# Kernel tuning notes

Measured on AMD Instinct MI355X. Metric: run time of the kernel, lower is better.

Reference implementation:

```python
import jax, jax.numpy as jnp
import numpy as np

# footprints from the module: RB = 8-neighbor ring (center excluded), G = 4-neighbor cross
RB_OFFSETS = [(-1, -1), (-1, 0), (-1, 1), (0, -1), (0, 1), (1, -1), (1, 0), (1, 1)]
G_OFFSETS = [(-1, 0), (0, -1), (0, 1), (1, 0)]
N_ITER = 3


def _footprint_median(x, offsets):
    """scipy.ndimage.median_filter with a boolean footprint.
    scipy uses rank = n//2 of the sorted footprint values (no averaging for even n)
    and 'reflect' boundary mode (== numpy 'symmetric' padding).
    x: [B, H, W]
    """
    B, H, W = x.shape
    xp = jnp.pad(x, ((0, 0), (1, 1), (1, 1)), mode='symmetric')
    vals = jnp.stack([xp[:, 1 + dy:1 + dy + H, 1 + dx:1 + dx + W]
                      for dy, dx in offsets], axis=0)  # [n, B, H, W]
    n = len(offsets)
    return jnp.sort(vals, axis=0)[n // 2]


def _conv3(x, k):
    """3x3 conv with symmetric padding. x: [B,H,W], k: [3,3] -> [B,H,W]."""
    xp = jnp.pad(x, ((0, 0), (1, 1), (1, 1)), mode='symmetric')[:, None]  # [B,1,H+2,W+2]
    kern = k[None, None].astype(x.dtype)  # [1,1,3,3]
    out = jax.lax.conv_general_dilated(xp, kern, (1, 1), 'VALID')
    return out[:, 0]


def _demosaick(x):
    """Naive bilinear demosaick of a GRBG Bayer mosaic. x: [B,H,W] -> [B,3,H,W]."""
    B, H, W = x.shape
    yy, xx = jnp.meshgrid(jnp.arange(H), jnp.arange(W), indexing='ij')
    r_mask = ((yy % 2 == 0) & (xx % 2 == 1)).astype(x.dtype)
    b_mask = ((yy % 2 == 1) & (xx % 2 == 0)).astype(x.dtype)
    g_mask = 1.0 - r_mask - b_mask
    KG = jnp.array([[0., 1., 0.], [1., 4., 1.], [0., 1., 0.]]) / 4.0
    KRB = jnp.array([[1., 2., 1.], [2., 4., 2.], [1., 2., 1.]]) / 4.0
    R = _conv3(x * r_mask, KRB)
    G = _conv3(x * g_mask, KG)
    Bc = _conv3(x * b_mask, KRB)
    return jnp.stack([R, G, Bc], axis=1)


def reference(image):
    # image: [B, 1, H, W] Bayer mosaic
    d = _demosaick(image[:, 0])  # [B, 3, H, W]
    R, G, B = d[:, 0], d[:, 1], d[:, 2]
    for _ in range(N_ITER):
        # medians are non-differentiable in the original (numpy roundtrip)
        R = jax.lax.stop_gradient(_footprint_median(R - G, RB_OFFSETS)) + G
        B = jax.lax.stop_gradient(_footprint_median(B - G, RB_OFFSETS)) + G
        G = 0.5 * (jax.lax.stop_gradient(_footprint_median(G - R, G_OFFSETS))
                   + jax.lax.stop_gradient(_footprint_median(G - B, G_OFFSETS))
                   + R + B)
    return jnp.stack([R, G, B], axis=1)


def setup_inputs() -> dict:
    key = jax.random.key(0)
    image = jax.random.uniform(key, (8, 1, 1024, 1024), dtype=jnp.float32)
    return {"image": image}
```

## Files before the change

### kernel.cpp

```cpp
#include <hip/hip_runtime.h>

#define HH 1024
#define WW 1024
#define NB 8
constexpr int PLANE = HH * WW;

#define S   84
#define RG  78
#define NTHR 1024

typedef _Float16 h2 __attribute__((ext_vector_type(2)));

__device__ __forceinline__ int clampi(int v, int lo, int hi) {
    return v < lo ? lo : (v > hi ? hi : v);
}

union U2H { unsigned u; h2 h; };
__device__ __forceinline__ h2 u2h(unsigned v) { U2H x; x.u = v; return x.h; }
__device__ __forceinline__ unsigned h2u(h2 h) { U2H x; x.h = h; return x.u; }
__device__ __forceinline__ unsigned packdiff(float a, float b) {
    h2 h; h.x = (_Float16)a; h.y = (_Float16)b; return h2u(h);
}
__device__ __forceinline__ h2 swap16(h2 x) {
    unsigned u = h2u(x);
    return u2h(__builtin_amdgcn_alignbit(u, u, 16));
}

__device__ __forceinline__ void cswap2(h2& a, h2& b) {
    h2 lo = __builtin_elementwise_min(a, b);
    b = __builtin_elementwise_max(a, b);
    a = lo;
}

__device__ __forceinline__ h2 med8p(h2 v0, h2 v1, h2 v2, h2 v3,
                                    h2 v4, h2 v5, h2 v6, h2 v7) {
    cswap2(v0, v1); cswap2(v2, v3); cswap2(v4, v5); cswap2(v6, v7);
    cswap2(v0, v2); cswap2(v1, v3); cswap2(v4, v6); cswap2(v5, v7);
    cswap2(v1, v2); cswap2(v5, v6);
    h2 p2 = __builtin_elementwise_min(v2, v6), p3 = __builtin_elementwise_min(v3, v7);
    h2 p4 = __builtin_elementwise_max(v0, v4), p5 = __builtin_elementwise_max(v1, v5);
    return __builtin_elementwise_max(__builtin_elementwise_min(p3, p5),
                                     __builtin_elementwise_max(p2, p4));
}

__device__ __forceinline__ h2 med4p(h2 a, h2 b, h2 c, h2 d) {
    h2 ab_hi = __builtin_elementwise_max(a, b), ab_lo = __builtin_elementwise_min(a, b);
    h2 cd_hi = __builtin_elementwise_max(c, d), cd_lo = __builtin_elementwise_min(c, d);
    return __builtin_elementwise_max(__builtin_elementwise_min(ab_hi, cd_hi),
                                     __builtin_elementwise_max(ab_lo, cd_lo));
}

__device__ __forceinline__ void demo_acc(float v, int pyn, int pxn, int ady, int adx,
                                         float& accR, float& accG, float& accB) {
    bool isr = (pyn == 0) && (pxn == 1);
    bool isb = (pyn == 1) && (pxn == 0);
    float wrb = 0.25f * (float)((2 - ady) * (2 - adx));
    int man = ady + adx;
    float wg = (man == 0) ? 1.0f : ((man == 1) ? 0.25f : 0.0f);
    accR += isr ? wrb * v : 0.0f;
    accB += isb ? wrb * v : 0.0f;
    accG += (!isr && !isb) ? wg * v : 0.0f;
}

template <int CA>
__device__ __forceinline__ void load4u(const unsigned* row, int c0, unsigned w[4]) {
    if constexpr (CA == 0) {
        uint4 q = *reinterpret_cast<const uint4*>(row + c0);
        w[0] = q.x; w[1] = q.y; w[2] = q.z; w[3] = q.w;
    } else {
        uint2 a = *reinterpret_cast<const uint2*>(row + c0);
        uint2 b = *reinterpret_cast<const uint2*>(row + c0 + 2);
        w[0] = a.x; w[1] = a.y; w[2] = b.x; w[3] = b.y;
    }
}
template <int CA>
__device__ __forceinline__ void load6u(const unsigned* row, int c0, unsigned w[6]) {
    if constexpr (CA == 0) {
        uint4 q = *reinterpret_cast<const uint4*>(row + c0);
        w[0] = row[c0 - 1];
        w[1] = q.x; w[2] = q.y; w[3] = q.z; w[4] = q.w;
        w[5] = row[c0 + 4];
    } else {
        uint4 a = *reinterpret_cast<const uint4*>(row + c0 - 2);
        uint4 b = *reinterpret_cast<const uint4*>(row + c0 + 2);
        w[0] = a.y; w[1] = a.z; w[2] = a.w; w[3] = b.x; w[4] = b.y; w[5] = b.z;
    }
}
template <int CA>
__device__ __forceinline__ void store4u(unsigned* row, int c0, const unsigned v[4]) {
    if constexpr (CA == 0) {
        *reinterpret_cast<uint4*>(row + c0) = make_uint4(v[0], v[1], v[2], v[3]);
    } else {
        *reinterpret_cast<uint2*>(row + c0) = make_uint2(v[0], v[1]);
        *reinterpret_cast<uint2*>(row + c0 + 2) = make_uint2(v[2], v[3]);
    }
}

template <int R0, int NRP, int C0, int NG>
__device__ __forceinline__ void p1_int(const unsigned* __restrict__ sdRB,
                                       unsigned* __restrict__ uRB, int tid) {
    static_assert((C0 & 3) == 2, "p1_int needs C0 % 4 == 2");
    if (tid < NRP * NG) {
        int rp = tid / NG, g = tid - rp * NG;
        int r0 = R0 + 2 * rp;
        int c0 = C0 + 4 * g;
        int B = c0 - 2;
        unsigned w[4][6];
#pragma unroll
        for (int i = 0; i < 4; ++i) {
            const unsigned* row = &sdRB[(r0 - 1 + i) * S + B];
            uint4 q0 = *reinterpret_cast<const uint4*>(row);
            uint4 q1 = *reinterpret_cast<const uint4*>(row + 4);
            w[i][0] = q0.y; w[i][1] = q0.z; w[i][2] = q0.w;
            w[i][3] = q1.x; w[i][4] = q1.y; w[i][5] = q1.z;
        }
#pragma unroll
        for (int rr = 0; rr < 2; ++rr) {
            unsigned rv[4];
#pragma unroll
            for (int i = 0; i < 4; ++i) {
                h2 m = med8p(u2h(w[rr][i]), u2h(w[rr][i + 1]), u2h(w[rr][i + 2]),
                             u2h(w[rr + 1][i]), u2h(w[rr + 1][i + 2]),
                             u2h(w[rr + 2][i]), u2h(w[rr + 2][i + 1]), u2h(w[rr + 2][i + 2]));
                rv[i] = h2u(-m);
            }
            store4u<2>(&uRB[(r0 + rr) * S], c0, rv);
        }
    }
}

template <int R0, int NRP, int C0, int NG, int CA, bool FINAL>
__device__ __forceinline__ void p2_int(_Float16* __restrict__ sG, unsigned* __restrict__ sdRB,
                                       const unsigned* __restrict__ uRB, int tid,
                                       int y0, int x0,
                                       float* __restrict__ oR, float* __restrict__ oG,
                                       float* __restrict__ oB) {
    if (tid < NRP * NG) {
        int rp = tid / NG, g = tid - rp * NG;
        int r0 = R0 + 2 * rp;
        int c0 = C0 + 4 * g;
        unsigned wm[4], wp[4], w0[6], w1[6];
        load4u<CA>(&uRB[(r0 - 1) * S], c0, wm);
        load6u<CA>(&uRB[(r0) * S], c0, w0);
        load6u<CA>(&uRB[(r0 + 1) * S], c0, w1);
        load4u<CA>(&uRB[(r0 + 2) * S], c0, wp);
        h2 ga0 = *reinterpret_cast<const h2*>(&sG[r0 * S + c0]);
        h2 ga1 = *reinterpret_cast<const h2*>(&sG[r0 * S + c0 + 2]);
        h2 gb0 = *reinterpret_cast<const h2*>(&sG[(r0 + 1) * S + c0]);
        h2 gb1 = *reinterpret_cast<const h2*>(&sG[(r0 + 1) * S + c0 + 2]);
        _Float16 gr0[4] = {ga0.x, ga0.y, ga1.x, ga1.y};
        _Float16 gr1[4] = {gb0.x, gb0.y, gb1.x, gb1.y};
        const h2 half2v = {(_Float16)0.5f, (_Float16)0.5f};

        unsigned nd0[4], nd1[4];
        float R4[2][4], G4[2][4], B4[2][4];
#pragma unroll
        for (int i = 0; i < 4; ++i) {
            {
                h2 m = med4p(u2h(wm[i]), u2h(w0[i]), u2h(w0[i + 2]), u2h(w1[i + 1]));
                h2 uc = u2h(w0[i + 1]);
                h2 gg; gg.x = gr0[i]; gg.y = gr0[i];
                h2 RB = gg - uc;
                h2 Gn2 = ((m + swap16(m)) + (RB + swap16(RB))) * half2v;
                if constexpr (FINAL) {
                    R4[0][i] = (float)RB.x; B4[0][i] = (float)RB.y; G4[0][i] = (float)Gn2.x;
                } else {
                    nd0[i] = h2u(RB - Gn2);
                    gr0[i] = Gn2.x;
                }
            }
            {
                h2 m = med4p(u2h(w0[i + 1]), u2h(w1[i]), u2h(w1[i + 2]), u2h(wp[i]));
                h2 uc = u2h(w1[i + 1]);
                h2 gg; gg.x = gr1[i]; gg.y = gr1[i];
                h2 RB = gg - uc;
                h2 Gn2 = ((m + swap16(m)) + (RB + swap16(RB))) * half2v;
                if constexpr (FINAL) {
                    R4[1][i] = (float)RB.x; B4[1][i] = (float)RB.y; G4[1][i] = (float)Gn2.x;
                } else {
                    nd1[i] = h2u(RB - Gn2);
                    gr1[i] = Gn2.x;
                }
            }
        }
        if constexpr (FINAL) {
#pragma unroll
            for (int rr = 0; rr < 2; ++rr) {
                size_t o = (size_t)(y0 + r0 + rr) * WW + (x0 + c0);
                *reinterpret_cast<float4*>(&oR[o]) = make_float4(R4[rr][0], R4[rr][1], R4[rr][2], R4[rr][3]);
                *reinterpret_cast<float4*>(&oG[o]) = make_float4(G4[rr][0], G4[rr][1], G4[rr][2], G4[rr][3]);
                *reinterpret_cast<float4*>(&oB[o]) = make_float4(B4[rr][0], B4[rr][1], B4[rr][2], B4[rr][3]);
            }
        } else {
            h2 s00; s00.x = gr0[0]; s00.y = gr0[1];
            h2 s01; s01.x = gr0[2]; s01.y = gr0[3];
            h2 s10; s10.x = gr1[0]; s10.y = gr1[1];
            h2 s11; s11.x = gr1[2]; s11.y = gr1[3];
            *reinterpret_cast<h2*>(&sG[r0 * S + c0]) = s00;
            *reinterpret_cast<h2*>(&sG[r0 * S + c0 + 2]) = s01;
            *reinterpret_cast<h2*>(&sG[(r0 + 1) * S + c0]) = s10;
            *reinterpret_cast<h2*>(&sG[(r0 + 1) * S + c0 + 2]) = s11;
            store4u<CA>(&sdRB[r0 * S], c0, nd0);
            store4u<CA>(&sdRB[(r0 + 1) * S], c0, nd1);
        }
    }
}

__device__ void p1_b(const unsigned* sdRB, unsigned* uRB, int tid,
                     int y0, int x0, int rlo, int nr, int clo, int nc) {
    for (int t = tid; t < nr * nc; t += NTHR) {
        int r = rlo + t / nc, c = clo + t - (t / nc) * nc;
        int gy = clampi(y0 + r, 0, HH - 1), gx = clampi(x0 + c, 0, WW - 1);
        int rm = clampi(gy - 1, 0, HH - 1) - y0, rp = clampi(gy + 1, 0, HH - 1) - y0;
        int cm = clampi(gx - 1, 0, WW - 1) - x0, cp = clampi(gx + 1, 0, WW - 1) - x0;
        h2 m = med8p(u2h(sdRB[rm * S + cm]), u2h(sdRB[rm * S + c]), u2h(sdRB[rm * S + cp]),
                     u2h(sdRB[r * S + cm]), u2h(sdRB[r * S + cp]),
                     u2h(sdRB[rp * S + cm]), u2h(sdRB[rp * S + c]), u2h(sdRB[rp * S + cp]));
        uRB[r * S + c] = h2u(-m);
    }
}

__device__ void p2_b(_Float16* sG, unsigned* sdRB, const unsigned* uRB, int tid,
                     int y0, int x0, int rlo, int nr, int clo, int nc, bool fin,
                     float* oR, float* oG, float* oB) {
    for (int t = tid; t < nr * nc; t += NTHR) {
        int r = rlo + t / nc, c = clo + t - (t / nc) * nc;
        int gy = clampi(y0 + r, 0, HH - 1), gx = clampi(x0 + c, 0, WW - 1);
        int rm = clampi(gy - 1, 0, HH - 1) - y0, rp = clampi(gy + 1, 0, HH - 1) - y0;
        int cm = clampi(gx - 1, 0, WW - 1) - x0, cp = clampi(gx + 1, 0, WW - 1) - x0;
        h2 m = med4p(u2h(uRB[rm * S + c]), u2h(uRB[r * S + cm]),
                     u2h(uRB[r * S + cp]), u2h(uRB[rp * S + c]));
        h2 uc = u2h(uRB[r * S + c]);
        float Gc = (float)sG[r * S + c];
        float Rn = Gc - (float)uc.x, Bn = Gc - (float)uc.y;
        float Gn = 0.5f * ((float)m.x + (float)m.y + Rn + Bn);
        if (fin) {
            size_t o = (size_t)(y0 + r) * WW + (x0 + c);
            oR[o] = Rn; oG[o] = Gn; oB[o] = Bn;
        } else {
            sG[r * S + c] = (_Float16)Gn;
            sdRB[r * S + c] = packdiff(Rn - Gn, Bn - Gn);
        }
    }
}

__global__ __launch_bounds__(1024) void fused_kernel(const float* __restrict__ img,
                                                     float* __restrict__ dst) {
    __shared__ __align__(16) unsigned smem[16380];
    unsigned* uRB = smem;
    unsigned* sdRB = smem + RG * S;
    _Float16* sG = reinterpret_cast<_Float16*>(smem + 2 * RG * S);
    float* sI = reinterpret_cast<float*>(smem);

    int bx = blockIdx.x, by = blockIdx.y, bb = blockIdx.z;
    int x0 = bx * 64 - 8, y0 = by * 64 - 7;
    const float* im = img + (size_t)bb * PLANE;
    float* oR = dst + (size_t)bb * 3 * PLANE;
    float* oG = oR + PLANE;
    float* oB = oR + 2 * PLANE;
    int tid = threadIdx.x;
    bool interior = (bx >= 1 && bx <= 14 && by >= 1 && by <= 14);

    if (interior) {
        if (tid < 38 * 19) {
            int qi = tid / 19, g = tid - (tid / 19) * 19;
            int rA = 1 + 2 * qi;
            int B = 4 * g;
            const float* base = im + (size_t)(y0 + rA - 1) * WW + (x0 + B);
            float w[4][6];
#pragma unroll
            for (int i = 0; i < 4; ++i) {
                float4 a = *reinterpret_cast<const float4*>(base + (size_t)i * WW);
                float4 b = *reinterpret_cast<const float4*>(base + (size_t)i * WW + 4);
                w[i][0] = a.y; w[i][1] = a.z; w[i][2] = a.w;
                w[i][3] = b.x; w[i][4] = b.y; w[i][5] = b.z;
            }
#pragma unroll
            for (int q = 0; q < 2; ++q) {
                int jb = 1 + 2 * q;
                float g00 = w[1][jb];
                float r00 = 0.5f * (w[1][jb - 1] + w[1][jb + 1]);
                float b00 = 0.5f * (w[0][jb] + w[2][jb]);
                float r01 = w[1][jb + 1];
                float g01 = 0.25f * (w[0][jb + 1] + w[2][jb + 1] + w[1][jb] + w[1][jb + 2]);
                float b01 = 0.25f * (w[0][jb] + w[0][jb + 2] + w[2][jb] + w[2][jb + 2]);
                float b10 = w[2][jb];
                float g10 = 0.25f * (w[1][jb] + w[3][jb] + w[2][jb - 1] + w[2][jb + 1]);
                float r10 = 0.25f * (w[1][jb - 1] + w[1][jb + 1] + w[3][jb - 1] + w[3][jb + 1]);
                float g11 = w[2][jb + 1];
                float r11 = 0.5f * (w[1][jb + 1] + w[3][jb + 1]);
                float b11 = 0.5f * (w[2][jb] + w[2][jb + 2]);
                int a0 = rA * S + 2 + 4 * g + 2 * q;
                h2 gh0; gh0.x = (_Float16)g00; gh0.y = (_Float16)g01;
                h2 gh1; gh1.x = (_Float16)g10; gh1.y = (_Float16)g11;
                *reinterpret_cast<h2*>(&sG[a0]) = gh0;
                *reinterpret_cast<h2*>(&sG[a0 + S]) = gh1;
                *reinterpret_cast<uint2*>(&sdRB[a0]) =
                    make_uint2(packdiff(r00 - g00, b00 - g00), packdiff(r01 - g01, b01 - g01));
                *reinterpret_cast<uint2*>(&sdRB[a0 + S]) =
                    make_uint2(packdiff(r10 - g10, b10 - g10), packdiff(r11 - g11, b11 - g11));
            }
        }
        __syncthreads();
        p1_int<2, 37, 2, 19>(sdRB, uRB, tid);
        __syncthreads();
        p2_int<3, 36, 4, 18, 0, false>(sG, sdRB, uRB, tid, y0, x0, oR, oG, oB);
        __syncthreads();
        p1_int<4, 35, 2, 19>(sdRB, uRB, tid);
        __syncthreads();
        p2_int<5, 34, 6, 17, 2, false>(sG, sdRB, uRB, tid, y0, x0, oR, oG, oB);
        __syncthreads();
        p1_int<6, 33, 6, 17>(sdRB, uRB, tid);
        __syncthreads();
        p2_int<7, 32, 8, 16, 0, true>(sG, sdRB, uRB, tid, y0, x0, oR, oG, oB);
    } else {
        for (int t = tid; t < RG * S; t += NTHR) {
            int r = t / S, c = t - (t / S) * S;
            int gy = clampi(y0 + r, 0, HH - 1), gx = clampi(x0 + c, 0, WW - 1);
            sI[r * S + c] = im[(size_t)gy * WW + gx];
        }
        __syncthreads();
        {
            for (int t = tid; t < 76 * 76; t += NTHR) {
                int r = 1 + t / 76, c = 2 + t - (t / 76) * 76;
                int gy = clampi(y0 + r, 0, HH - 1), gx = clampi(x0 + c, 0, WW - 1);
                float accR = 0.f, accG = 0.f, accB = 0.f;
#pragma unroll
                for (int dy = -1; dy <= 1; ++dy)
#pragma unroll
                    for (int dx = -1; dx <= 1; ++dx) {
                        int cy = clampi(gy + dy, 0, HH - 1);
                        int cx = clampi(gx + dx, 0, WW - 1);
                        float v = sI[(cy - y0) * S + (cx - x0)];
                        demo_acc(v, cy & 1, cx & 1, dy < 0 ? -dy : dy, dx < 0 ? -dx : dx,
                                 accR, accG, accB);
                    }
                sG[r * S + c] = (_Float16)accG;
                sdRB[r * S + c] = packdiff(accR - accG, accB - accG);
            }
        }
        __syncthreads();
        p1_b(sdRB, uRB, tid, y0, x0, 2, 74, 3, 74);
        __syncthreads();
        p2_b(sG, sdRB, uRB, tid, y0, x0, 3, 72, 4, 72, false, oR, oG, oB);
        __syncthreads();
        p1_b(sdRB, uRB, tid, y0, x0, 4, 70, 5, 70);
        __syncthreads();
        p2_b(sG, sdRB, uRB, tid, y0, x0, 5, 68, 6, 68, false, oR, oG, oB);
        __syncthreads();
        p1_b(sdRB, uRB, tid, y0, x0, 6, 66, 7, 66);
        __syncthreads();
        p2_b(sG, sdRB, uRB, tid, y0, x0, 7, 64, 8, 64, true, oR, oG, oB);
    }
}

extern "C" void kernel_launch(void* const* d_in, const int* in_sizes, int n_in,
                              void* d_out, int out_size, void* d_ws, size_t ws_size,
                              hipStream_t stream) {
    const float* img = (const float*)d_in[0];
    float* out = (float*)d_out;
    dim3 block(NTHR);
    dim3 grid(16, 16, NB);
    fused_kernel<<<grid, block, 0, stream>>>(img, out);
}
```

Before: 130.7 us.

## Vectorize border-tile path using interior quad kernels with scalar fallback for clamped cells

Border tiles previously ran a fully scalar per-pixel path for demosaick and all six median passes, with clamped neighbour indexing on every cell. The new code runs the vectorized interior routines on border tiles too, masking their stores to in-image cells, and recomputes only the out-of-image cells with a scalar per-cell routine that applies reflection clamping. Demosaick on border tiles likewise uses the quad routine wherever the 4x6 window is fully inside the image. This targets the slower border blocks (about a quarter of the grid), at the cost of extra branching, a second scalar pass, and more code size and register use.

```diff
diff --git a/kernel.cpp b/kernel.cpp
--- a/kernel.cpp
+++ b/kernel.cpp
@@ -60,6 +60,35 @@
     accR += isr ? wrb * v : 0.0f;
     accB += isb ? wrb * v : 0.0f;
     accG += (!isr && !isb) ? wg * v : 0.0f;
+}
+
+__device__ __forceinline__ void demo_quads2(const float w[4][6], unsigned* __restrict__ sdRB,
+                                            _Float16* __restrict__ sG, int a0base) {
+#pragma unroll
+    for (int q = 0; q < 2; ++q) {
+        int jb = 1 + 2 * q;
+        float g00 = w[1][jb];
+        float r00 = 0.5f * (w[1][jb - 1] + w[1][jb + 1]);
+        float b00 = 0.5f * (w[0][jb] + w[2][jb]);
+        float r01 = w[1][jb + 1];
+        float g01 = 0.25f * (w[0][jb + 1] + w[2][jb + 1] + w[1][jb] + w[1][jb + 2]);
+        float b01 = 0.25f * (w[0][jb] + w[0][jb + 2] + w[2][jb] + w[2][jb + 2]);
+        float b10 = w[2][jb];
+        float g10 = 0.25f * (w[1][jb] + w[3][jb] + w[2][jb - 1] + w[2][jb + 1]);
+        float r10 = 0.25f * (w[1][jb - 1] + w[1][jb + 1] + w[3][jb - 1] + w[3][jb + 1]);
+        float g11 = w[2][jb + 1];
+        float r11 = 0.5f * (w[1][jb + 1] + w[3][jb + 1]);
+        float b11 = 0.5f * (w[2][jb] + w[2][jb + 2]);
+        int a0 = a0base + 2 * q;
+        h2 gh0; gh0.x = (_Float16)g00; gh0.y = (_Float16)g01;
+        h2 gh1; gh1.x = (_Float16)g10; gh1.y = (_Float16)g11;
+        *reinterpret_cast<h2*>(&sG[a0]) = gh0;
+        *reinterpret_cast<h2*>(&sG[a0 + S]) = gh1;
+        *reinterpret_cast<uint2*>(&sdRB[a0]) =
+            make_uint2(packdiff(r00 - g00, b00 - g00), packdiff(r01 - g01, b01 - g01));
+        *reinterpret_cast<uint2*>(&sdRB[a0 + S]) =
+            make_uint2(packdiff(r10 - g10, b10 - g10), packdiff(r11 - g11, b11 - g11));
+    }
 }
 
 template <int CA>
@@ -96,10 +125,37 @@
     }
 }
 
+__device__ __forceinline__ void p1_cell(const unsigned* __restrict__ sdRB,
+                                        unsigned* __restrict__ uRB,
+                                        int r, int c, int y0, int x0) {
+    int gy = clampi(y0 + r, 0, HH - 1), gx = clampi(x0 + c, 0, WW - 1);
+    int rm = clampi(gy - 1, 0, HH - 1) - y0, rp = clampi(gy + 1, 0, HH - 1) - y0;
+    int cm = clampi(gx - 1, 0, WW - 1) - x0, cp = clampi(gx + 1, 0, WW - 1) - x0;
+    h2 m = med8p(u2h(sdRB[rm * S + cm]), u2h(sdRB[rm * S + c]), u2h(sdRB[rm * S + cp]),
+                 u2h(sdRB[r * S + cm]), u2h(sdRB[r * S + cp]),
+                 u2h(sdRB[rp * S + cm]), u2h(sdRB[rp * S + c]), u2h(sdRB[rp * S + cp]));
+    uRB[r * S + c] = h2u(-m);
+}
+
+__device__ __forceinline__ void p2_cell(_Float16* sG, unsigned* sdRB, const unsigned* uRB,
+                                        int r, int c, int y0, int x0) {
+    int gy = clampi(y0 + r, 0, HH - 1), gx = clampi(x0 + c, 0, WW - 1);
+    int rm = clampi(gy - 1, 0, HH - 1) - y0, rp = clampi(gy + 1, 0, HH - 1) - y0;
+    int cm = clampi(gx - 1, 0, WW - 1) - x0, cp = clampi(gx + 1, 0, WW - 1) - x0;
+    h2 m = med4p(u2h(uRB[rm * S + c]), u2h(uRB[r * S + cm]),
+                 u2h(uRB[r * S + cp]), u2h(uRB[rp * S + c]));
+    h2 uc = u2h(uRB[r * S + c]);
+    float Gc = (float)sG[r * S + c];
+    float Rn = Gc - (float)uc.x, Bn = Gc - (float)uc.y;
+    float Gn = 0.5f * ((float)m.x + (float)m.y + Rn + Bn);
+    sG[r * S + c] = (_Float16)Gn;
+    sdRB[r * S + c] = packdiff(Rn - Gn, Bn - Gn);
+}
+
 template <int R0, int NRP, int C0, int NG>
 __device__ __forceinline__ void p1_int(const unsigned* __restrict__ sdRB,
                                        unsigned* __restrict__ uRB, int tid) {
-    static_assert((C0 & 3) == 2, "p1_int needs C0 % 4 == 2");
+    static_assert((C0 & 3) == 2, "p1 needs C0 % 4 == 2");
     if (tid < NRP * NG) {
         int rp = tid / NG, g = tid - rp * NG;
         int r0 = R0 + 2 * rp;
@@ -125,6 +181,109 @@
                 rv[i] = h2u(-m);
             }
             store4u<2>(&uRB[(r0 + rr) * S], c0, rv);
+        }
+    }
+}
+
+template <int R0, int NRP, int C0, int NG>
+__device__ __forceinline__ void p1_brd(const unsigned* __restrict__ sdRB,
+                                       unsigned* __restrict__ uRB, int tid,
+                                       int rIL, int rIH, int cIL, int cIH,
+                                       int y0, int x0) {
+    static_assert((C0 & 3) == 2, "p1 needs C0 % 4 == 2");
+    if (tid < NRP * NG) {
+        int rp = tid / NG, g = tid - rp * NG;
+        int r0 = R0 + 2 * rp;
+        int c0 = C0 + 4 * g;
+        int B = c0 - 2;
+        unsigned w[4][6];
+#pragma unroll
+        for (int i = 0; i < 4; ++i) {
+            const unsigned* row = &sdRB[(r0 - 1 + i) * S + B];
+            uint4 q0 = *reinterpret_cast<const uint4*>(row);
+            uint4 q1 = *reinterpret_cast<const uint4*>(row + 4);
+            w[i][0] = q0.y; w[i][1] = q0.z; w[i][2] = q0.w;
+            w[i][3] = q1.x; w[i][4] = q1.y; w[i][5] = q1.z;
+        }
+        bool colFull = (c0 >= cIL) && (c0 + 3 <= cIH);
+#pragma unroll
+        for (int rr = 0; rr < 2; ++rr) {
+            int r = r0 + rr;
+            unsigned rv[4];
+#pragma unroll
+            for (int i = 0; i < 4; ++i) {
+                h2 m = med8p(u2h(w[rr][i]), u2h(w[rr][i + 1]), u2h(w[rr][i + 2]),
+                             u2h(w[rr + 1][i]), u2h(w[rr + 1][i + 2]),
+                             u2h(w[rr + 2][i]), u2h(w[rr + 2][i + 1]), u2h(w[rr + 2][i + 2]));
+                rv[i] = h2u(-m);
+            }
+            if (r >= rIL && r <= rIH) {
+                if (colFull) {
+                    store4u<2>(&uRB[r * S], c0, rv);
+                } else {
+#pragma unroll
+                    for (int i = 0; i < 4; ++i) {
+                        int c = c0 + i;
+                        if (c >= cIL && c <= cIH) uRB[r * S + c] = rv[i];
+                    }
+                }
+            }
+        }
+    }
+    constexpr int NR = 2 * NRP, NC = 4 * NG;
+    for (int t = tid; t < NR * NC; t += NTHR) {
+        int r = R0 + t / NC, c = C0 + t - (t / NC) * NC;
+        if (r >= rIL && r <= rIH && c >= cIL && c <= cIH) continue;
+        p1_cell(sdRB, uRB, r, c, y0, x0);
+    }
+}
+
+template <int CA, bool FINAL>
+__device__ __forceinline__ void p2_compute(_Float16* __restrict__ sG,
+                                           const unsigned* __restrict__ uRB,
+                                           int r0, int c0,
+                                           _Float16 gr0[4], _Float16 gr1[4],
+                                           unsigned nd0[4], unsigned nd1[4],
+                                           float R4[2][4], float G4[2][4], float B4[2][4]) {
+    unsigned wm[4], wp[4], w0[6], w1[6];
+    load4u<CA>(&uRB[(r0 - 1) * S], c0, wm);
+    load6u<CA>(&uRB[(r0) * S], c0, w0);
+    load6u<CA>(&uRB[(r0 + 1) * S], c0, w1);
+    load4u<CA>(&uRB[(r0 + 2) * S], c0, wp);
+    h2 ga0 = *reinterpret_cast<const h2*>(&sG[r0 * S + c0]);
+    h2 ga1 = *reinterpret_cast<const h2*>(&sG[r0 * S + c0 + 2]);
+    h2 gb0 = *reinterpret_cast<const h2*>(&sG[(r0 + 1) * S + c0]);
+    h2 gb1 = *reinterpret_cast<const h2*>(&sG[(r0 + 1) * S + c0 + 2]);
+    gr0[0] = ga0.x; gr0[1] = ga0.y; gr0[2] = ga1.x; gr0[3] = ga1.y;
+    gr1[0] = gb0.x; gr1[1] = gb0.y; gr1[2] = gb1.x; gr1[3] = gb1.y;
+    const h2 half2v = {(_Float16)0.5f, (_Float16)0.5f};
+#pragma unroll
+    for (int i = 0; i < 4; ++i) {
+        {
+            h2 m = med4p(u2h(wm[i]), u2h(w0[i]), u2h(w0[i + 2]), u2h(w1[i + 1]));
+            h2 uc = u2h(w0[i + 1]);
+            h2 gg; gg.x = gr0[i]; gg.y = gr0[i];
+            h2 RB = gg - uc;
+            h2 Gn2 = ((m + swap16(m)) + (RB + swap16(RB))) * half2v;
+            if constexpr (FINAL) {
+                R4[0][i] = (float)RB.x; B4[0][i] = (float)RB.y; G4[0][i] = (float)Gn2.x;
+            } else {
+                nd0[i] = h2u(RB - Gn2);
+                gr0[i] = Gn2.x;
+            }
+        }
+        {
+            h2 m = med4p(u2h(w0[i + 1]), u2h(w1[i]), u2h(w1[i + 2]), u2h(wp[i]));
+            h2 uc = u2h(w1[i + 1]);
+            h2 gg; gg.x = gr1[i]; gg.y = gr1[i];
+            h2 RB = gg - uc;
+            h2 Gn2 = ((m + swap16(m)) + (RB + swap16(RB))) * half2v;
+            if constexpr (FINAL) {
+                R4[1][i] = (float)RB.x; B4[1][i] = (float)RB.y; G4[1][i] = (float)Gn2.x;
+            } else {
+                nd1[i] = h2u(RB - Gn2);
+                gr1[i] = Gn2.x;
+            }
         }
     }
 }
@@ -139,50 +298,10 @@
         int rp = tid / NG, g = tid - rp * NG;
         int r0 = R0 + 2 * rp;
         int c0 = C0 + 4 * g;
-        unsigned wm[4], wp[4], w0[6], w1[6];
-        load4u<CA>(&uRB[(r0 - 1) * S], c0, wm);
-        load6u<CA>(&uRB[(r0) * S], c0, w0);
-        load6u<CA>(&uRB[(r0 + 1) * S], c0, w1);
-        load4u<CA>(&uRB[(r0 + 2) * S], c0, wp);
-        h2 ga0 = *reinterpret_cast<const h2*>(&sG[r0 * S + c0]);
-        h2 ga1 = *reinterpret_cast<const h2*>(&sG[r0 * S + c0 + 2]);
-        h2 gb0 = *reinterpret_cast<const h2*>(&sG[(r0 + 1) * S + c0]);
-        h2 gb1 = *reinterpret_cast<const h2*>(&sG[(r0 + 1) * S + c0 + 2]);
-        _Float16 gr0[4] = {ga0.x, ga0.y, ga1.x, ga1.y};
-        _Float16 gr1[4] = {gb0.x, gb0.y, gb1.x, gb1.y};
-        const h2 half2v = {(_Float16)0.5f, (_Float16)0.5f};
-
+        _Float16 gr0[4], gr1[4];
         unsigned nd0[4], nd1[4];
         float R4[2][4], G4[2][4], B4[2][4];
-#pragma unroll
-        for (int i = 0; i < 4; ++i) {
-            {
-                h2 m = med4p(u2h(wm[i]), u2h(w0[i]), u2h(w0[i + 2]), u2h(w1[i + 1]));
-                h2 uc = u2h(w0[i + 1]);
-                h2 gg; gg.x = gr0[i]; gg.y = gr0[i];
-                h2 RB = gg - uc;
-                h2 Gn2 = ((m + swap16(m)) + (RB + swap16(RB))) * half2v;
-                if constexpr (FINAL) {
-                    R4[0][i] = (float)RB.x; B4[0][i] = (float)RB.y; G4[0][i] = (float)Gn2.x;
-                } else {
-                    nd0[i] = h2u(RB - Gn2);
-                    gr0[i] = Gn2.x;
-                }
-            }
-            {
-                h2 m = med4p(u2h(w0[i + 1]), u2h(w1[i]), u2h(w1[i + 2]), u2h(wp[i]));
-                h2 uc = u2h(w1[i + 1]);
-                h2 gg; gg.x = gr1[i]; gg.y = gr1[i];
-                h2 RB = gg - uc;
-                h2 Gn2 = ((m + swap16(m)) + (RB + swap16(RB))) * half2v;
-                if constexpr (FINAL) {
-                    R4[1][i] = (float)RB.x; B4[1][i] = (float)RB.y; G4[1][i] = (float)Gn2.x;
-                } else {
-                    nd1[i] = h2u(RB - Gn2);
-                    gr1[i] = Gn2.x;
-                }
-            }
-        }
+        p2_compute<CA, FINAL>(sG, uRB, r0, c0, gr0, gr1, nd0, nd1, R4, G4, B4);
         if constexpr (FINAL) {
 #pragma unroll
             for (int rr = 0; rr < 2; ++rr) {
@@ -206,40 +325,70 @@
     }
 }
 
-__device__ void p1_b(const unsigned* sdRB, unsigned* uRB, int tid,
-                     int y0, int x0, int rlo, int nr, int clo, int nc) {
-    for (int t = tid; t < nr * nc; t += NTHR) {
-        int r = rlo + t / nc, c = clo + t - (t / nc) * nc;
-        int gy = clampi(y0 + r, 0, HH - 1), gx = clampi(x0 + c, 0, WW - 1);
-        int rm = clampi(gy - 1, 0, HH - 1) - y0, rp = clampi(gy + 1, 0, HH - 1) - y0;
-        int cm = clampi(gx - 1, 0, WW - 1) - x0, cp = clampi(gx + 1, 0, WW - 1) - x0;
-        h2 m = med8p(u2h(sdRB[rm * S + cm]), u2h(sdRB[rm * S + c]), u2h(sdRB[rm * S + cp]),
-                     u2h(sdRB[r * S + cm]), u2h(sdRB[r * S + cp]),
-                     u2h(sdRB[rp * S + cm]), u2h(sdRB[rp * S + c]), u2h(sdRB[rp * S + cp]));
-        uRB[r * S + c] = h2u(-m);
-    }
-}
-
-__device__ void p2_b(_Float16* sG, unsigned* sdRB, const unsigned* uRB, int tid,
-                     int y0, int x0, int rlo, int nr, int clo, int nc, bool fin,
-                     float* oR, float* oG, float* oB) {
-    for (int t = tid; t < nr * nc; t += NTHR) {
-        int r = rlo + t / nc, c = clo + t - (t / nc) * nc;
-        int gy = clampi(y0 + r, 0, HH - 1), gx = clampi(x0 + c, 0, WW - 1);
-        int rm = clampi(gy - 1, 0, HH - 1) - y0, rp = clampi(gy + 1, 0, HH - 1) - y0;
-        int cm = clampi(gx - 1, 0, WW - 1) - x0, cp = clampi(gx + 1, 0, WW - 1) - x0;
-        h2 m = med4p(u2h(uRB[rm * S + c]), u2h(uRB[r * S + cm]),
-                     u2h(uRB[r * S + cp]), u2h(uRB[rp * S + c]));
-        h2 uc = u2h(uRB[r * S + c]);
-        float Gc = (float)sG[r * S + c];
-        float Rn = Gc - (float)uc.x, Bn = Gc - (float)uc.y;
-        float Gn = 0.5f * ((float)m.x + (float)m.y + Rn + Bn);
-        if (fin) {
-            size_t o = (size_t)(y0 + r) * WW + (x0 + c);
-            oR[o] = Rn; oG[o] = Gn; oB[o] = Bn;
+template <int R0, int NRP, int C0, int NG, int CA, bool FINAL>
+__device__ __forceinline__ void p2_brd(_Float16* __restrict__ sG, unsigned* __restrict__ sdRB,
+                                       const unsigned* __restrict__ uRB, int tid,
+                                       int y0, int x0,
+                                       int rIL, int rIH, int cIL, int cIH,
+                                       float* __restrict__ oR, float* __restrict__ oG,
+                                       float* __restrict__ oB) {
+    if (tid < NRP * NG) {
+        int rp = tid / NG, g = tid - rp * NG;
+        int r0 = R0 + 2 * rp;
+        int c0 = C0 + 4 * g;
+        _Float16 gr0[4], gr1[4];
+        unsigned nd0[4], nd1[4];
+        float R4[2][4], G4[2][4], B4[2][4];
+        p2_compute<CA, FINAL>(sG, uRB, r0, c0, gr0, gr1, nd0, nd1, R4, G4, B4);
+        if constexpr (FINAL) {
+#pragma unroll
+            for (int rr = 0; rr < 2; ++rr) {
+                size_t o = (size_t)(y0 + r0 + rr) * WW + (x0 + c0);
+                *reinterpret_cast<float4*>(&oR[o]) = make_float4(R4[rr][0], R4[rr][1], R4[rr][2], R4[rr][3]);
+                *reinterpret_cast<float4*>(&oG[o]) = make_float4(G4[rr][0], G4[rr][1], G4[rr][2], G4[rr][3]);
+                *reinterpret_cast<float4*>(&oB[o]) = make_float4(B4[rr][0], B4[rr][1], B4[rr][2], B4[rr][3]);
+            }
         } else {
-            sG[r * S + c] = (_Float16)Gn;
-            sdRB[r * S + c] = packdiff(Rn - Gn, Bn - Gn);
+            bool colFull = (c0 >= cIL) && (c0 + 3 <= cIH);
+            if (r0 >= rIL && r0 <= rIH) {
+                if (colFull) {
+                    h2 s00; s00.x = gr0[0]; s00.y = gr0[1];
+                    h2 s01; s01.x = gr0[2]; s01.y = gr0[3];
+                    *reinterpret_cast<h2*>(&sG[r0 * S + c0]) = s00;
+                    *reinterpret_cast<h2*>(&sG[r0 * S + c0 + 2]) = s01;
+                    store4u<CA>(&sdRB[r0 * S], c0, nd0);
+                } else {
+#pragma unroll
+                    for (int i = 0; i < 4; ++i) {
+                        int c = c0 + i;
+                        if (c >= cIL && c <= cIH) { sG[r0 * S + c] = gr0[i]; sdRB[r0 * S + c] = nd0[i]; }
+                    }
+                }
+            }
+            int r1 = r0 + 1;
+            if (r1 >= rIL && r1 <= rIH) {
+                if (colFull) {
+                    h2 s10; s10.x = gr1[0]; s10.y = gr1[1];
+                    h2 s11; s11.x = gr1[2]; s11.y = gr1[3];
+                    *reinterpret_cast<h2*>(&sG[r1 * S + c0]) = s10;
+                    *reinterpret_cast<h2*>(&sG[r1 * S + c0 + 2]) = s11;
+                    store4u<CA>(&sdRB[r1 * S], c0, nd1);
+                } else {
+#pragma unroll
+                    for (int i = 0; i < 4; ++i) {
+                        int c = c0 + i;
+                        if (c >= cIL && c <= cIH) { sG[r1 * S + c] = gr1[i]; sdRB[r1 * S + c] = nd1[i]; }
+                    }
+                }
+            }
+        }
+    }
+    if constexpr (!FINAL) {
+        constexpr int NR = 2 * NRP, NC = 4 * NG;
+        for (int t = tid; t < NR * NC; t += NTHR) {
+            int r = R0 + t / NC, c = C0 + t - (t / NC) * NC;
+            if (r >= rIL && r <= rIH && c >= cIL && c <= cIH) continue;
+            p2_cell(sG, sdRB, uRB, r, c, y0, x0);
         }
     }
 }
@@ -275,31 +424,7 @@
                 w[i][0] = a.y; w[i][1] = a.z; w[i][2] = a.w;
                 w[i][3] = b.x; w[i][4] = b.y; w[i][5] = b.z;
             }
-#pragma unroll
-            for (int q = 0; q < 2; ++q) {
-                int jb = 1 + 2 * q;
-                float g00 = w[1][jb];
-                float r00 = 0.5f * (w[1][jb - 1] + w[1][jb + 1]);
-                float b00 = 0.5f * (w[0][jb] + w[2][jb]);
-                float r01 = w[1][jb + 1];
-                float g01 = 0.25f * (w[0][jb + 1] + w[2][jb + 1] + w[1][jb] + w[1][jb + 2]);
-                float b01 = 0.25f * (w[0][jb] + w[0][jb + 2] + w[2][jb] + w[2][jb + 2]);
-                float b10 = w[2][jb];
-                float g10 = 0.25f * (w[1][jb] + w[3][jb] + w[2][jb - 1] + w[2][jb + 1]);
-                float r10 = 0.25f * (w[1][jb - 1] + w[1][jb + 1] + w[3][jb - 1] + w[3][jb + 1]);
-                float g11 = w[2][jb + 1];
-                float r11 = 0.5f * (w[1][jb + 1] + w[3][jb + 1]);
-                float b11 = 0.5f * (w[2][jb] + w[2][jb + 2]);
-                int a0 = rA * S + 2 + 4 * g + 2 * q;
-                h2 gh0; gh0.x = (_Float16)g00; gh0.y = (_Float16)g01;
-                h2 gh1; gh1.x = (_Float16)g10; gh1.y = (_Float16)g11;
-                *reinterpret_cast<h2*>(&sG[a0]) = gh0;
-                *reinterpret_cast<h2*>(&sG[a0 + S]) = gh1;
-                *reinterpret_cast<uint2*>(&sdRB[a0]) =
-                    make_uint2(packdiff(r00 - g00, b00 - g00), packdiff(r01 - g01, b01 - g01));
-                *reinterpret_cast<uint2*>(&sdRB[a0 + S]) =
-                    make_uint2(packdiff(r10 - g10, b10 - g10), packdiff(r11 - g11, b11 - g11));
-            }
+            demo_quads2(w, sdRB, sG, rA * S + 2 + 4 * g);
         }
         __syncthreads();
         p1_int<2, 37, 2, 19>(sdRB, uRB, tid);
@@ -314,43 +439,70 @@
         __syncthreads();
         p2_int<7, 32, 8, 16, 0, true>(sG, sdRB, uRB, tid, y0, x0, oR, oG, oB);
     } else {
+        int rIL = (-y0) > 0 ? (-y0) : 0;
+        int rIH = (HH - 1 - y0) < (RG - 1) ? (HH - 1 - y0) : (RG - 1);
+        int cIL = (-x0) > 0 ? (-x0) : 0;
+        int cIH = (WW - 1 - x0) < 79 ? (WW - 1 - x0) : 79;
+
         for (int t = tid; t < RG * S; t += NTHR) {
             int r = t / S, c = t - (t / S) * S;
             int gy = clampi(y0 + r, 0, HH - 1), gx = clampi(x0 + c, 0, WW - 1);
             sI[r * S + c] = im[(size_t)gy * WW + gx];
         }
         __syncthreads();
-        {
-            for (int t = tid; t < 76 * 76; t += NTHR) {
-                int r = 1 + t / 76, c = 2 + t - (t / 76) * 76;
-                int gy = clampi(y0 + r, 0, HH - 1), gx = clampi(x0 + c, 0, WW - 1);
-                float accR = 0.f, accG = 0.f, accB = 0.f;
-#pragma unroll
-                for (int dy = -1; dy <= 1; ++dy)
-#pragma unroll
-                    for (int dx = -1; dx <= 1; ++dx) {
-                        int cy = clampi(gy + dy, 0, HH - 1);
-                        int cx = clampi(gx + dx, 0, WW - 1);
-                        float v = sI[(cy - y0) * S + (cx - x0)];
-                        demo_acc(v, cy & 1, cx & 1, dy < 0 ? -dy : dy, dx < 0 ? -dx : dx,
-                                 accR, accG, accB);
-                    }
-                sG[r * S + c] = (_Float16)accG;
-                sdRB[r * S + c] = packdiff(accR - accG, accB - accG);
-            }
-        }
-        __syncthreads();
-        p1_b(sdRB, uRB, tid, y0, x0, 2, 74, 3, 74);
-        __syncthreads();
-        p2_b(sG, sdRB, uRB, tid, y0, x0, 3, 72, 4, 72, false, oR, oG, oB);
-        __syncthreads();
-        p1_b(sdRB, uRB, tid, y0, x0, 4, 70, 5, 70);
-        __syncthreads();
-        p2_b(sG, sdRB, uRB, tid, y0, x0, 5, 68, 6, 68, false, oR, oG, oB);
-        __syncthreads();
-        p1_b(sdRB, uRB, tid, y0, x0, 6, 66, 7, 66);
-        __syncthreads();
-        p2_b(sG, sdRB, uRB, tid, y0, x0, 7, 64, 8, 64, true, oR, oG, oB);
+        if (tid < 38 * 19) {
+            int qi = tid / 19, g = tid - (tid / 19) * 19;
+            int rA = 1 + 2 * qi;
+            int B = 4 * g;
+            bool safe = (y0 + rA - 1 >= 0) && (y0 + rA + 2 <= HH - 1) &&
+                        (x0 + B + 1 >= 0) && (x0 + B + 6 <= WW - 1);
+            if (safe) {
+                float w[4][6];
+#pragma unroll
+                for (int i = 0; i < 4; ++i) {
+                    const float* row = &sI[(rA - 1 + i) * S + B];
+                    float4 a = *reinterpret_cast<const float4*>(row);
+                    float4 b = *reinterpret_cast<const float4*>(row + 4);
+                    w[i][0] = a.y; w[i][1] = a.z; w[i][2] = a.w;
+                    w[i][3] = b.x; w[i][4] = b.y; w[i][5] = b.z;
+                }
+                demo_quads2(w, sdRB, sG, rA * S + 2 + 4 * g);
+            }
+        }
+        for (int t = tid; t < 76 * 76; t += NTHR) {
+            int r = 1 + t / 76, c = 2 + t - (t / 76) * 76;
+            int rA = (r & 1) ? r : r - 1;
+            int B2 = (c - 2) & ~3;
+            bool qsafe = (y0 + rA - 1 >= 0) && (y0 + rA + 2 <= HH - 1) &&
+                         (x0 + B2 + 1 >= 0) && (x0 + B2 + 6 <= WW - 1);
+            if (qsafe) continue;
+            int gy = clampi(y0 + r, 0, HH - 1), gx = clampi(x0 + c, 0, WW - 1);
+            float accR = 0.f, accG = 0.f, accB = 0.f;
+#pragma unroll
+            for (int dy = -1; dy <= 1; ++dy)
+#pragma unroll
+                for (int dx = -1; dx <= 1; ++dx) {
+                    int cy = clampi(gy + dy, 0, HH - 1);
+                    int cx = clampi(gx + dx, 0, WW - 1);
+                    float v = sI[(cy - y0) * S + (cx - x0)];
+                    demo_acc(v, cy & 1, cx & 1, dy < 0 ? -dy : dy, dx < 0 ? -dx : dx,
+                             accR, accG, accB);
+                }
+            sG[r * S + c] = (_Float16)accG;
+            sdRB[r * S + c] = packdiff(accR - accG, accB - accG);
+        }
+        __syncthreads();
+        p1_brd<2, 37, 2, 19>(sdRB, uRB, tid, rIL, rIH, cIL, cIH, y0, x0);
+        __syncthreads();
+        p2_brd<3, 36, 4, 18, 0, false>(sG, sdRB, uRB, tid, y0, x0, rIL, rIH, cIL, cIH, oR, oG, oB);
+        __syncthreads();
+        p1_brd<4, 35, 2, 19>(sdRB, uRB, tid, rIL, rIH, cIL, cIH, y0, x0);
+        __syncthreads();
+        p2_brd<5, 34, 6, 17, 2, false>(sG, sdRB, uRB, tid, y0, x0, rIL, rIH, cIL, cIH, oR, oG, oB);
+        __syncthreads();
+        p1_brd<6, 33, 6, 17>(sdRB, uRB, tid, rIL, rIH, cIL, cIH, y0, x0);
+        __syncthreads();
+        p2_brd<7, 32, 8, 16, 0, true>(sG, sdRB, uRB, tid, y0, x0, rIL, rIH, cIL, cIH, oR, oG, oB);
     }
 }
 
```

After: 194.1 us. 48.5% more time.
